# Performance work log

Measured on AMD Instinct MI355X. Metric: run time of the kernel, lower is better.

Reference implementation:

```python
import jax, jax.numpy as jnp
import numpy as np

B, L, S, E, H, Z = 512, 128, 64, 256, 256, 64

def _ln(x, g, b):
    m = jnp.mean(x, -1, keepdims=True)
    v = jnp.mean((x - m) ** 2, -1, keepdims=True)
    return (x - m) / jnp.sqrt(v + 1e-5) * g + b

def _gru_layer(x, Wih, Whh, bih, bhh):
    # x: (B, T, in) -> (outputs (B, T, H), last hidden (B, H)); torch nn.GRU gate math
    xg = jnp.swapaxes(jnp.einsum('bti,gi->btg', x, Wih) + bih, 0, 1)  # (T, B, 3H) precomputed input gates
    h0 = jnp.zeros((x.shape[0], Whh.shape[1]), x.dtype)
    def step(h, xg_t):
        hg = h @ Whh.T + bhh
        xr, xz, xn = jnp.split(xg_t, 3, -1)
        hr, hz, hn = jnp.split(hg, 3, -1)
        r = jax.nn.sigmoid(xr + hr)
        zg = jax.nn.sigmoid(xz + hz)
        n = jnp.tanh(xn + r * hn)
        h_new = (1.0 - zg) * n + zg * h
        return h_new, h_new
    hT, ys = jax.lax.scan(step, h0, xg)
    return jnp.swapaxes(ys, 0, 1), hT

def setup_inputs() -> dict:
    key = jax.random.key(0)
    ks = iter(jax.random.split(key, 64))
    def u(shape, fan):
        s = 1.0 / np.sqrt(fan)
        return jax.random.uniform(next(ks), shape, jnp.float32, -s, s)
    inp = {
        'x': jax.random.normal(next(ks), (B, L, S), jnp.float32),
        'eps': jax.random.normal(next(ks), (B, Z), jnp.float32),
        'dec_noise': jax.random.normal(next(ks), (B, L, Z), jnp.float32),
        'in_W': u((E, S), S), 'in_b': u((E,), S),
        'in_g': jnp.ones((E,), jnp.float32), 'in_beta': jnp.zeros((E,), jnp.float32),
        'eW0i': u((3 * H, E), H), 'eW0h': u((3 * H, H), H), 'eb0i': u((3 * H,), H), 'eb0h': u((3 * H,), H),
        'eW1i': u((3 * H, H), H), 'eW1h': u((3 * H, H), H), 'eb1i': u((3 * H,), H), 'eb1h': u((3 * H,), H),
        'mu_W': u((Z, H), H), 'mu_b': u((Z,), H), 'lv_W': u((Z, H), H), 'lv_b': u((Z,), H),
        'dW0i': u((3 * H, Z), H), 'dW0h': u((3 * H, H), H), 'db0i': u((3 * H,), H), 'db0h': u((3 * H,), H),
        'dW1i': u((3 * H, H), H), 'dW1h': u((3 * H, H), H), 'db1i': u((3 * H,), H), 'db1h': u((3 * H,), H),
        'post_W': u((H, H), H), 'post_b': u((H,), H),
        'post_g': jnp.ones((H,), jnp.float32), 'post_beta': jnp.zeros((H,), jnp.float32),
        'out_W': u((S, H), H), 'out_b': u((S,), H),
    }
    return inp

def reference(x, eps, dec_noise, in_W, in_b, in_g, in_beta,
              eW0i, eW0h, eb0i, eb0h, eW1i, eW1h, eb1i, eb1h,
              mu_W, mu_b, lv_W, lv_b,
              dW0i, dW0h, db0i, db0h, dW1i, dW1h, db1i, db1h,
              post_W, post_b, post_g, post_beta, out_W, out_b):
    # encode
    h = _ln(jax.nn.relu(x @ in_W.T + in_b), in_g, in_beta)          # input_proj
    h, _ = _gru_layer(h, eW0i, eW0h, eb0i, eb0h)                    # encoder GRU layer 0
    _, h_last = _gru_layer(h, eW1i, eW1h, eb1i, eb1h)               # encoder GRU layer 1, h_n[-1]
    mu = h_last @ mu_W.T + mu_b
    log_var = h_last @ lv_W.T + lv_b
    z = mu + eps * jnp.exp(0.5 * log_var)                           # reparameterize
    # decode
    z_seq = jnp.broadcast_to(z[:, None, :], (z.shape[0], L, Z)) + dec_noise * 0.05
    d, _ = _gru_layer(z_seq, dW0i, dW0h, db0i, db0h)
    d, _ = _gru_layer(d, dW1i, dW1h, db1i, db1h)
    d = _ln(jax.nn.relu(d @ post_W.T + post_b), post_g, post_beta)  # post_rnn_proj
    x_hat = jnp.tanh(d @ out_W.T + out_b)                           # output_layer
    return (x_hat, mu, log_var)
```

## Files before the change

kernel.cpp:

```cpp
#include <hip/hip_runtime.h>
#include <hip/hip_bf16.h>
#include <stdint.h>

#define DEVI static __device__ __forceinline__

typedef __bf16 bf16x8 __attribute__((ext_vector_type(8)));
typedef float f32x4 __attribute__((ext_vector_type(4)));
typedef int   int4v __attribute__((ext_vector_type(4)));
typedef int   int2v __attribute__((ext_vector_type(2)));

DEVI float bf2f(uint16_t u){ uint32_t x = ((uint32_t)u) << 16; float f; __builtin_memcpy(&f, &x, 4); return f; }
DEVI uint16_t f2bf(float f){ uint32_t u; __builtin_memcpy(&u, &f, 4); uint32_t r = (u + 0x7FFFu + ((u >> 16) & 1u)) >> 16; return (uint16_t)r; }
DEVI float frcp(float x){ return __builtin_amdgcn_rcpf(x); }
DEVI float sigm(float x){ return frcp(1.f + __expf(-x)); }
DEVI float tanhfast(float x){ return 1.f - 2.f * frcp(1.f + __expf(2.f * x)); }
DEVI f32x4 mfma16(bf16x8 a, bf16x8 b, f32x4 c){ return __builtin_amdgcn_mfma_f32_16x16x32_bf16(a, b, c, 0, 0, 0); }

DEVI bf16x8 cvt8(const float* __restrict__ p){
    f32x4 a = *(const f32x4*)p, b = *(const f32x4*)(p + 4);
    union { bf16x8 v; uint16_t u[8]; } r;
    #pragma unroll
    for (int e = 0; e < 4; ++e) { r.u[e] = f2bf(a[e]); r.u[4 + e] = f2bf(b[e]); }
    return r.v;
}
DEVI int4v asint4(bf16x8 v){ int4v r; __builtin_memcpy(&r, &v, 16); return r; }

DEVI void bar_lds(){
    asm volatile("s_waitcnt lgkmcnt(0)" ::: "memory");
    __builtin_amdgcn_s_barrier();
    __builtin_amdgcn_sched_barrier(0);
}


__global__ __launch_bounds__(256) void k_inproj(
    const float* __restrict__ X, const float* __restrict__ W,
    const float* __restrict__ bias, const float* __restrict__ g,
    const float* __restrict__ beta, uint16_t* __restrict__ Y)
{
    __shared__ __align__(16) char As[64 * 128];
    __shared__ __align__(16) char Bs[256 * 128];
    __shared__ __align__(16) char Cs[64 * 520];
    const int tid = threadIdx.x;
    const long rowbase = (long)blockIdx.x * 64;

    #pragma unroll
    for (int it = 0; it < 2; ++it) {
        int c = it * 256 + tid; int r = c >> 3, cc = c & 7;
        bf16x8 v = cvt8(X + (rowbase + r) * 64 + cc * 8);
        *(int4v*)(As + r * 128 + ((cc * 16) ^ ((r & 7) << 4))) = asint4(v);
    }
    #pragma unroll
    for (int it = 0; it < 8; ++it) {
        int c = it * 256 + tid; int r = c >> 3, cc = c & 7;
        bf16x8 v = cvt8(W + r * 64 + cc * 8);
        *(int4v*)(Bs + r * 128 + ((cc * 16) ^ ((r & 7) << 4))) = asint4(v);
    }
    __syncthreads();

    const int w = tid >> 6, l = tid & 63, lr = l & 15, lg = l >> 4;
    f32x4 acc[16];
    #pragma unroll
    for (int i = 0; i < 16; ++i) acc[i] = (f32x4){0.f, 0.f, 0.f, 0.f};
    const int arow = w * 16 + lr;
    #pragma unroll
    for (int ks = 0; ks < 2; ++ks) {
        bf16x8 a = *(bf16x8*)(As + arow * 128 + ((ks * 64 + lg * 16) ^ ((arow & 7) << 4)));
        #pragma unroll
        for (int tl = 0; tl < 16; ++tl) {
            int n = tl * 16 + lr;
            bf16x8 b = *(bf16x8*)(Bs + n * 128 + ((ks * 64 + lg * 16) ^ ((n & 7) << 4)));
            acc[tl] = mfma16(a, b, acc[tl]);
        }
    }
    float gv[16], bv[16], biasv[16];
    #pragma unroll
    for (int tl = 0; tl < 16; ++tl) {
        int col = tl * 16 + lr;
        gv[tl] = g[col]; bv[tl] = beta[col]; biasv[tl] = bias[col];
    }
    #pragma unroll
    for (int i = 0; i < 4; ++i) {
        float s = 0.f, sq = 0.f, v[16];
        #pragma unroll
        for (int tl = 0; tl < 16; ++tl) {
            float xv = acc[tl][i] + biasv[tl]; xv = fmaxf(xv, 0.f);
            v[tl] = xv; s += xv; sq += xv * xv;
        }
        #pragma unroll
        for (int d = 1; d < 16; d <<= 1) { s += __shfl_xor(s, d); sq += __shfl_xor(sq, d); }
        float mean = s * (1.f / 256.f);
        float var  = sq * (1.f / 256.f) - mean * mean;
        float sc   = rsqrtf(var + 1e-5f);
        int rl = w * 16 + lg * 4 + i;
        #pragma unroll
        for (int tl = 0; tl < 16; ++tl)
            *(uint16_t*)(Cs + rl * 520 + (tl * 16 + lr) * 2) =
                f2bf((v[tl] - mean) * sc * gv[tl] + bv[tl]);
    }
    __syncthreads();
    #pragma unroll
    for (int it = 0; it < 16; ++it) {
        int idx = it * 256 + tid;
        int rl = idx >> 6, ch = idx & 63;
        long rg = rowbase + rl;
        long ri = ((rg & 127) << 9) + (rg >> 7);
        *(int2v*)(Y + ri * 256 + ch * 4) = *(int2v*)(Cs + rl * 520 + ch * 8);
    }
}

template<int KIN, bool ZBUILD>
__global__ __launch_bounds__(512) void k_xg(
    const uint16_t* __restrict__ A, const float* __restrict__ W,
    const float* __restrict__ bias, uint16_t* __restrict__ XG,
    const float* __restrict__ zbuf, const float* __restrict__ noise)
{
    constexpr int KB = KIN * 2;
    constexpr int KS = KIN / 32;
    __shared__ __align__(16) char Bs[192 * KB];
    __shared__ __align__(16) char Cs[128 * 400];
    const int tid = threadIdx.x;
    const int nb = blockIdx.y;

    constexpr int CPR = KIN / 8;
    for (int c = tid; c < 192 * CPR; c += 512) {
        int r = c / CPR, cc = c % CPR;
        bf16x8 v = cvt8(W + (long)(nb * 192 + r) * KIN + cc * 8);
        *(int4v*)(Bs + r * KB + ((cc * 16) ^ ((r & 7) << 4))) = asint4(v);
    }
    __syncthreads();

    const int w = tid >> 6, l = tid & 63, lr = l & 15, lg = l >> 4;
    float bvs[12];
    #pragma unroll
    for (int tl = 0; tl < 12; ++tl) bvs[tl] = bias[nb * 192 + tl * 16 + lr];

    for (int rt = 0; rt < 8; ++rt) {
        const long rowb = (long)blockIdx.x * 1024 + rt * 128;
        const long ria  = rowb + w * 16 + lr;
        bf16x8 a[KS];
        if constexpr (!ZBUILD) {
            #pragma unroll
            for (int ks = 0; ks < KS; ++ks)
                a[ks] = *(const bf16x8*)(A + ria * KIN + ks * 32 + lg * 8);
        } else {
            int b = (int)(ria & 511), t = (int)(ria >> 9);
            #pragma unroll
            for (int ks = 0; ks < KS; ++ks) {
                int k0 = ks * 32 + lg * 8;
                const float* zr = zbuf + b * 64 + k0;
                const float* nr = noise + ((long)b * 128 + t) * 64 + k0;
                f32x4 z0 = *(const f32x4*)zr, z1 = *(const f32x4*)(zr + 4);
                f32x4 n0 = *(const f32x4*)nr, n1 = *(const f32x4*)(nr + 4);
                union { bf16x8 v; uint16_t u[8]; } un;
                #pragma unroll
                for (int e = 0; e < 4; ++e) {
                    un.u[e]     = f2bf(z0[e] + 0.05f * n0[e]);
                    un.u[4 + e] = f2bf(z1[e] + 0.05f * n1[e]);
                }
                a[ks] = un.v;
            }
        }
        f32x4 acc[12];
        #pragma unroll
        for (int i = 0; i < 12; ++i) acc[i] = (f32x4){0.f, 0.f, 0.f, 0.f};
        #pragma unroll
        for (int ks = 0; ks < KS; ++ks) {
            #pragma unroll
            for (int tl = 0; tl < 12; ++tl) {
                int n = tl * 16 + lr;
                bf16x8 b = *(bf16x8*)(Bs + n * KB + ((ks * 64 + lg * 16) ^ ((n & 7) << 4)));
                acc[tl] = mfma16(a[ks], b, acc[tl]);
            }
        }
        #pragma unroll
        for (int tl = 0; tl < 12; ++tl) {
            #pragma unroll
            for (int i = 0; i < 4; ++i)
                *(uint16_t*)(Cs + (w * 16 + lg * 4 + i) * 400 + (tl * 16 + lr) * 2) =
                    f2bf(acc[tl][i] + bvs[tl]);
        }
        __syncthreads();
        #pragma unroll
        for (int it = 0; it < 6; ++it) {
            int idx = it * 512 + tid;
            int row = idx / 24, ch = idx % 24;
            *(int4v*)(XG + (rowb + row) * 768 + nb * 192 + ch * 8) =
                *(int4v*)(Cs + row * 400 + ch * 16);
        }
        __syncthreads();
    }
}

__global__ __launch_bounds__(512) void k_gru(
    const uint16_t* __restrict__ XG, const float* __restrict__ Whh,
    const float* __restrict__ bhh, uint16_t* __restrict__ Y,
    float* __restrict__ hlast)
{
    constexpr int L = 128;
    __shared__ __align__(16) char Abuf[2][2 * 512];
    __shared__ __align__(16) char Wt[768 * 72 + 8];
    const int tid = threadIdx.x;
    const int w = tid >> 6, l = tid & 63, lr = l & 15, lg = l >> 4;
    const int rowg0 = blockIdx.x * 2;

    ((uint32_t*)Abuf)[tid] = 0;

    #pragma unroll
    for (int it = 0; it < 6; ++it) {
        int c = it * 512 + tid; int r = c >> 2, cc = c & 3;
        bf16x8 v = cvt8(Whh + (long)r * 256 + 224 + cc * 8);
        *(int4v*)(Wt + r * 72 + cc * 16) = asint4(v);
    }

    int gb[6];
    #pragma unroll
    for (int tl = 0; tl < 6; ++tl) gb[tl] = (tl >> 1) * 256 + w * 32 + (tl & 1) * 16;
    bf16x8 wf[6][7];
    #pragma unroll
    for (int tl = 0; tl < 6; ++tl)
        #pragma unroll
        for (int ks = 0; ks < 7; ++ks)
            wf[tl][ks] = cvt8(Whh + (long)(gb[tl] + lr) * 256 + ks * 32 + lg * 8);

    const int i_  = lg & 1;
    const int sub = (lg >> 1) & 1;
    const int col = w * 32 + sub * 16 + lr;
    const float bR = bhh[col], bZ = bhh[256 + col], bN = bhh[512 + col];
    const long rowl = rowg0 + i_;
    const int wrbyte = i_ * 512 + ((((col * 2) & ~15) ^ (i_ << 6)) | ((col * 2) & 15));

    uint16_t xga0 = XG[rowl * 768 + col];
    uint16_t xga1 = XG[rowl * 768 + 256 + col];
    uint16_t xga2 = XG[rowl * 768 + 512 + col];
    float h = 0.f;
    const bool wy = (Y != nullptr);
    const int arow = lr & 1;
    __syncthreads();

    for (int t = 0; t < L; ++t) {
        const int p = t & 1;
        f32x4 acc[6];
        #pragma unroll
        for (int i = 0; i < 6; ++i) acc[i] = (f32x4){0.f, 0.f, 0.f, 0.f};

        const char* ab = Abuf[p];
        bf16x8 aq[4];
        #pragma unroll
        for (int i = 0; i < 4; ++i)
            aq[i] = *(bf16x8*)(ab + arow * 512 + ((i * 64 + lg * 16) ^ (arow << 6)));
        #pragma unroll
        for (int ks = 0; ks < 8; ++ks) {
            bf16x8 acur = aq[ks & 3];
            if (ks + 4 < 8)
                aq[ks & 3] = *(bf16x8*)(ab + arow * 512 + (((ks + 4) * 64 + lg * 16) ^ (arow << 6)));
            if (ks < 7) {
                #pragma unroll
                for (int tl = 0; tl < 6; ++tl) acc[tl] = mfma16(acur, wf[tl][ks], acc[tl]);
            } else {
                #pragma unroll
                for (int tl = 0; tl < 6; ++tl) {
                    bf16x8 b = *(bf16x8*)(Wt + (gb[tl] + lr) * 72 + lg * 16);
                    acc[tl] = mfma16(acur, b, acc[tl]);
                }
            }
        }

        float pre0, pre1, pre2;
        {
            float a0 = i_ ? acc[0][1] : acc[0][0];
            float a1 = i_ ? acc[1][1] : acc[1][0];
            pre0 = sub ? a1 : a0;
            float b0 = i_ ? acc[2][1] : acc[2][0];
            float b1 = i_ ? acc[3][1] : acc[3][0];
            pre1 = sub ? b1 : b0;
            float c0 = i_ ? acc[4][1] : acc[4][0];
            float c1 = i_ ? acc[5][1] : acc[5][0];
            pre2 = sub ? c1 : c0;
        }
        float xr = bf2f(xga0), xz = bf2f(xga1), xn = bf2f(xga2);
        float R = sigm(xr + pre0 + bR);
        float Z = sigm(xz + pre1 + bZ);
        float N = tanhfast(xn + R * (pre2 + bN));
        h = N + Z * (h - N);
        uint16_t hb = f2bf(h);
        *(uint16_t*)(Abuf[p ^ 1] + wrbyte) = hb;

        if (t + 1 < L) {
            const uint16_t* src = XG + ((long)(t + 1) * 512 + rowl) * 768;
            xga0 = src[col]; xga1 = src[256 + col]; xga2 = src[512 + col];
        }
        if (wy) Y[((long)t * 512 + rowl) * 256 + col] = hb;
        bar_lds();
    }
    if (hlast) hlast[rowl * 256 + col] = h;
}

__global__ __launch_bounds__(256) void k_z(
    const float* __restrict__ hlast, const float* __restrict__ muW,
    const float* __restrict__ mub, const float* __restrict__ lvW,
    const float* __restrict__ lvb, const float* __restrict__ eps,
    float* __restrict__ mu_out, float* __restrict__ lv_out,
    float* __restrict__ zout)
{
    __shared__ float hrow[2][256];
    __shared__ float res[2][128];
    const int tid = threadIdx.x;
    const long row0 = (long)blockIdx.x * 2;
    for (int i = tid; i < 512; i += 256) ((float*)hrow)[i] = hlast[row0 * 256 + i];
    __syncthreads();
    const int lrr = tid >> 7, c = tid & 127;
    const float* Wr = (c < 64 ? muW : lvW) + (long)(c & 63) * 256;
    float acc = (c < 64) ? mub[c] : lvb[c & 63];
    const float* hr = hrow[lrr];
    #pragma unroll 8
    for (int k = 0; k < 256; k += 4) {
        f32x4 wv = *(const f32x4*)(Wr + k);
        #pragma unroll
        for (int e = 0; e < 4; ++e) acc += hr[k + e] * wv[e];
    }
    res[lrr][c] = acc;
    long row = row0 + lrr;
    if (c < 64) mu_out[row * 64 + c] = acc;
    else        lv_out[row * 64 + (c & 63)] = acc;
    __syncthreads();
    if (c < 64) {
        float m = res[lrr][c], lv = res[lrr][64 + c];
        zout[row * 64 + c] = m + eps[row * 64 + c] * __expf(0.5f * lv);
    }
}

__global__ __launch_bounds__(256) void k_post(
    const uint16_t* __restrict__ D1, const float* __restrict__ pW,
    const float* __restrict__ pb, const float* __restrict__ pg,
    const float* __restrict__ pbeta, const float* __restrict__ oW,
    const float* __restrict__ ob, float* __restrict__ xhat)
{
    __shared__ __align__(16) char Bs[256 * 512];
    const int tid = threadIdx.x;
    const long rowbase = (long)blockIdx.x * 64;
    #pragma unroll
    for (int it = 0; it < 32; ++it) {
        int c = it * 256 + tid; int r = c >> 5, cc = c & 31;
        bf16x8 v = cvt8(pW + r * 256 + cc * 8);
        *(int4v*)(Bs + r * 512 + ((cc * 16) ^ ((r & 7) << 4))) = asint4(v);
    }
    __syncthreads();
    const int w = tid >> 6, l = tid & 63, lr = l & 15, lg = l >> 4;
    const long arow = rowbase + w * 16 + lr;
    bf16x8 af[8];
    #pragma unroll
    for (int ks = 0; ks < 8; ++ks) af[ks] = *(const bf16x8*)(D1 + arow * 256 + ks * 32 + lg * 8);
    f32x4 acc[16];
    #pragma unroll
    for (int i = 0; i < 16; ++i) acc[i] = (f32x4){0.f, 0.f, 0.f, 0.f};
    #pragma unroll
    for (int ks = 0; ks < 8; ++ks) {
        #pragma unroll
        for (int tl = 0; tl < 16; ++tl) {
            int n = tl * 16 + lr;
            bf16x8 b = *(bf16x8*)(Bs + n * 512 + ((ks * 64 + lg * 16) ^ ((n & 7) << 4)));
            acc[tl] = mfma16(af[ks], b, acc[tl]);
        }
    }
    float gv[16], bv[16], biasv[16];
    #pragma unroll
    for (int tl = 0; tl < 16; ++tl) {
        int col = tl * 16 + lr;
        gv[tl] = pg[col]; bv[tl] = pbeta[col]; biasv[tl] = pb[col];
    }
    uint16_t dl[16][4];
    #pragma unroll
    for (int i = 0; i < 4; ++i) {
        float s = 0.f, sq = 0.f, v[16];
        #pragma unroll
        for (int tl = 0; tl < 16; ++tl) {
            float xv = acc[tl][i] + biasv[tl]; xv = fmaxf(xv, 0.f);
            v[tl] = xv; s += xv; sq += xv * xv;
        }
        #pragma unroll
        for (int d = 1; d < 16; d <<= 1) { s += __shfl_xor(s, d); sq += __shfl_xor(sq, d); }
        float mean = s * (1.f / 256.f);
        float var  = sq * (1.f / 256.f) - mean * mean;
        float sc   = rsqrtf(var + 1e-5f);
        #pragma unroll
        for (int tl = 0; tl < 16; ++tl)
            dl[tl][i] = f2bf((v[tl] - mean) * sc * gv[tl] + bv[tl]);
    }
    __syncthreads();
    #pragma unroll
    for (int tl = 0; tl < 16; ++tl) {
        int col = tl * 16 + lr;
        #pragma unroll
        for (int i = 0; i < 4; ++i) {
            int row = w * 16 + lg * 4 + i;
            *(uint16_t*)(Bs + row * 512 + (((col * 2) & ~15) ^ ((row & 7) << 4)) + ((col * 2) & 15)) = dl[tl][i];
        }
    }
    __syncthreads();
    const int ar2 = w * 16 + lr;
    f32x4 acc2[4];
    #pragma unroll
    for (int i = 0; i < 4; ++i) acc2[i] = (f32x4){0.f, 0.f, 0.f, 0.f};
    #pragma unroll
    for (int ks = 0; ks < 8; ++ks) {
        bf16x8 a = *(bf16x8*)(Bs + ar2 * 512 + ((ks * 64 + lg * 16) ^ ((ar2 & 7) << 4)));
        #pragma unroll
        for (int tl = 0; tl < 4; ++tl) {
            int n = tl * 16 + lr;
            bf16x8 b = cvt8(oW + n * 256 + ks * 32 + lg * 8);
            acc2[tl] = mfma16(a, b, acc2[tl]);
        }
    }
    #pragma unroll
    for (int tl = 0; tl < 4; ++tl) {
        int col = tl * 16 + lr;
        float bo = ob[col];
        #pragma unroll
        for (int i = 0; i < 4; ++i) {
            long ri = rowbase + w * 16 + lg * 4 + i;
            long b = ri & 511, t = ri >> 9;
            xhat[(b * 128 + t) * 64 + col] = tanhfast(acc2[tl][i] + bo);
        }
    }
}

extern "C" void kernel_launch(void* const* d_in, const int* in_sizes, int n_in,
                              void* d_out, int out_size, void* d_ws, size_t ws_size,
                              hipStream_t stream)
{
    (void)in_sizes; (void)n_in; (void)out_size; (void)ws_size;
    const float* x     = (const float*)d_in[0];
    const float* eps   = (const float*)d_in[1];
    const float* dnz   = (const float*)d_in[2];
    const float* in_W  = (const float*)d_in[3];
    const float* in_b  = (const float*)d_in[4];
    const float* in_g  = (const float*)d_in[5];
    const float* in_be = (const float*)d_in[6];
    const float* eW0i  = (const float*)d_in[7];
    const float* eW0h  = (const float*)d_in[8];
    const float* eb0i  = (const float*)d_in[9];
    const float* eb0h  = (const float*)d_in[10];
    const float* eW1i  = (const float*)d_in[11];
    const float* eW1h  = (const float*)d_in[12];
    const float* eb1i  = (const float*)d_in[13];
    const float* eb1h  = (const float*)d_in[14];
    const float* mu_W  = (const float*)d_in[15];
    const float* mu_b  = (const float*)d_in[16];
    const float* lv_W  = (const float*)d_in[17];
    const float* lv_b  = (const float*)d_in[18];
    const float* dW0i  = (const float*)d_in[19];
    const float* dW0h  = (const float*)d_in[20];
    const float* db0i  = (const float*)d_in[21];
    const float* db0h  = (const float*)d_in[22];
    const float* dW1i  = (const float*)d_in[23];
    const float* dW1h  = (const float*)d_in[24];
    const float* db1i  = (const float*)d_in[25];
    const float* db1h  = (const float*)d_in[26];
    const float* postW = (const float*)d_in[27];
    const float* postb = (const float*)d_in[28];
    const float* postg = (const float*)d_in[29];
    const float* postbe= (const float*)d_in[30];
    const float* outW  = (const float*)d_in[31];
    const float* outb  = (const float*)d_in[32];

    char* ws = (char*)d_ws;
    uint16_t* XG   = (uint16_t*)(ws);
    uint16_t* YA   = (uint16_t*)(ws + 100663296);
    uint16_t* YB   = (uint16_t*)(ws + 134217728);
    float*    hlast= (float*)   (ws + 167772160);
    float*    zbuf = (float*)   (ws + 168296448);

    float* out    = (float*)d_out;
    float* mu_out = out + 4194304;
    float* lv_out = out + 4194304 + 32768;

    dim3 b256(256), b512(512);
    dim3 gxg(64, 4);

    k_inproj<<<1024, b256, 0, stream>>>(x, in_W, in_b, in_g, in_be, YA);
    k_xg<256,false><<<gxg, b512, 0, stream>>>(YA, eW0i, eb0i, XG, nullptr, nullptr);
    k_gru<<<256, b512, 0, stream>>>(XG, eW0h, eb0h, YB, nullptr);
    k_xg<256,false><<<gxg, b512, 0, stream>>>(YB, eW1i, eb1i, XG, nullptr, nullptr);
    k_gru<<<256, b512, 0, stream>>>(XG, eW1h, eb1h, nullptr, hlast);
    k_z<<<256, b256, 0, stream>>>(hlast, mu_W, mu_b, lv_W, lv_b, eps, mu_out, lv_out, zbuf);
    k_xg<64,true><<<gxg, b512, 0, stream>>>(nullptr, dW0i, db0i, XG, zbuf, dnz);
    k_gru<<<256, b512, 0, stream>>>(XG, dW0h, db0h, YA, nullptr);
    k_xg<256,false><<<gxg, b512, 0, stream>>>(YA, dW1i, db1i, XG, nullptr, nullptr);
    k_gru<<<256, b512, 0, stream>>>(XG, dW1h, db1h, YB, nullptr);
    k_post<<<1024, b256, 0, stream>>>(YB, postW, postb, postg, postbe, outW, outb, out);
}
```

Measured before the change: 955.1 us.

## Add register-resident 4-wave GRU kernel for encoder and fold r/z hidden biases

Adds k_gru4, a 256-thread GRU recurrence kernel that keeps the whole recurrent weight matrix in registers (12x8 bf16 fragments per lane) and computes two hidden columns per lane. This removes the LDS-resident weight slice and its per-step LDS reads that k_gru uses. The encoder layers switch to it, while the decoder layers keep k_gru. Separately, the r and z hidden biases are folded into the precomputed input-gate bias, which saves two adds per step. The cost is very high register pressure with one wave per EU, and only 4 waves per block to hide per-step latency.

```diff
diff --git a/kernel.cpp b/kernel.cpp
--- a/kernel.cpp
+++ b/kernel.cpp
@@ -111,7 +111,8 @@
 template<int KIN, bool ZBUILD>
 __global__ __launch_bounds__(512) void k_xg(
     const uint16_t* __restrict__ A, const float* __restrict__ W,
-    const float* __restrict__ bias, uint16_t* __restrict__ XG,
+    const float* __restrict__ bias, const float* __restrict__ bhh,
+    uint16_t* __restrict__ XG,
     const float* __restrict__ zbuf, const float* __restrict__ noise)
 {
     constexpr int KB = KIN * 2;
@@ -132,7 +133,10 @@
     const int w = tid >> 6, l = tid & 63, lr = l & 15, lg = l >> 4;
     float bvs[12];
     #pragma unroll
-    for (int tl = 0; tl < 12; ++tl) bvs[tl] = bias[nb * 192 + tl * 16 + lr];
+    for (int tl = 0; tl < 12; ++tl) {
+        int colg = nb * 192 + tl * 16 + lr;
+        bvs[tl] = bias[colg] + (colg < 512 ? bhh[colg] : 0.f);
+    }
 
     for (int rt = 0; rt < 8; ++rt) {
         const long rowb = (long)blockIdx.x * 1024 + rt * 128;
@@ -191,6 +195,97 @@
     }
 }
 
+__global__ __launch_bounds__(256)
+__attribute__((amdgpu_waves_per_eu(1, 1)))
+void k_gru4(
+    const uint16_t* __restrict__ XG, const float* __restrict__ Whh,
+    const float* __restrict__ bhh, uint16_t* __restrict__ Y,
+    float* __restrict__ hlast)
+{
+    constexpr int L = 128;
+    __shared__ __align__(16) char Abuf[2][2 * 512];
+    const int tid = threadIdx.x;
+    const int w = tid >> 6, l = tid & 63, lr = l & 15, lg = l >> 4;
+    const int rowg0 = blockIdx.x * 2;
+
+    ((uint32_t*)Abuf)[tid] = 0;
+    ((uint32_t*)Abuf)[256 + tid] = 0;
+
+    int gb[12];
+    #pragma unroll
+    for (int tl = 0; tl < 12; ++tl) gb[tl] = (tl >> 2) * 256 + w * 64 + (tl & 3) * 16;
+    bf16x8 wf[12][8];
+    #pragma unroll
+    for (int tl = 0; tl < 12; ++tl)
+        #pragma unroll
+        for (int ks = 0; ks < 8; ++ks)
+            wf[tl][ks] = cvt8(Whh + (long)(gb[tl] + lr) * 256 + ks * 32 + lg * 8);
+
+    const int row = lg & 1;
+    const int hi  = (lg >> 1) & 1;
+    const int col0 = w * 64 + hi * 32 + lr;
+    const int col1 = col0 + 16;
+    const long rowl = rowg0 + row;
+    const float bN0 = bhh[512 + col0], bN1 = bhh[512 + col1];
+    const int wr0 = row * 512 + ((((col0 * 2) & ~15) ^ (row << 6)) | ((col0 * 2) & 15));
+    const int wr1 = row * 512 + ((((col1 * 2) & ~15) ^ (row << 6)) | ((col1 * 2) & 15));
+
+    uint16_t xr0 = XG[rowl * 768 + col0], xz0 = XG[rowl * 768 + 256 + col0], xn0 = XG[rowl * 768 + 512 + col0];
+    uint16_t xr1 = XG[rowl * 768 + col1], xz1 = XG[rowl * 768 + 256 + col1], xn1 = XG[rowl * 768 + 512 + col1];
+    float h0 = 0.f, h1 = 0.f;
+    const bool wy = (Y != nullptr);
+    const int arow = lr & 1;
+    __syncthreads();
+
+    for (int t = 0; t < L; ++t) {
+        const int p = t & 1;
+        const char* ab = Abuf[p];
+        f32x4 acc[12];
+        #pragma unroll
+        for (int i = 0; i < 12; ++i) acc[i] = (f32x4){0.f, 0.f, 0.f, 0.f};
+        #pragma unroll
+        for (int ks = 0; ks < 8; ++ks) {
+            bf16x8 a = *(bf16x8*)(ab + arow * 512 + ((ks * 64 + lg * 16) ^ (arow << 6)));
+            #pragma unroll
+            for (int tl = 0; tl < 12; ++tl) acc[tl] = mfma16(a, wf[tl][ks], acc[tl]);
+        }
+
+        #define SELG(tA, tB) (hi ? (row ? acc[tB][1] : acc[tB][0]) \
+                                 : (row ? acc[tA][1] : acc[tA][0]))
+        float pR0 = SELG(0, 2),  pR1 = SELG(1, 3);
+        float pZ0 = SELG(4, 6),  pZ1 = SELG(5, 7);
+        float pN0 = SELG(8, 10), pN1 = SELG(9, 11);
+        #undef SELG
+
+        float R0 = sigm(bf2f(xr0) + pR0);
+        float Z0 = sigm(bf2f(xz0) + pZ0);
+        float N0 = tanhfast(bf2f(xn0) + R0 * (pN0 + bN0));
+        h0 = N0 + Z0 * (h0 - N0);
+        float R1 = sigm(bf2f(xr1) + pR1);
+        float Z1 = sigm(bf2f(xz1) + pZ1);
+        float N1 = tanhfast(bf2f(xn1) + R1 * (pN1 + bN1));
+        h1 = N1 + Z1 * (h1 - N1);
+        uint16_t hb0 = f2bf(h0), hb1 = f2bf(h1);
+        *(uint16_t*)(Abuf[p ^ 1] + wr0) = hb0;
+        *(uint16_t*)(Abuf[p ^ 1] + wr1) = hb1;
+
+        if (t + 1 < L) {
+            const uint16_t* src = XG + ((long)(t + 1) * 512 + rowl) * 768;
+            xr0 = src[col0]; xz0 = src[256 + col0]; xn0 = src[512 + col0];
+            xr1 = src[col1]; xz1 = src[256 + col1]; xn1 = src[512 + col1];
+        }
+        if (wy) {
+            uint16_t* yd = Y + ((long)t * 512 + rowl) * 256;
+            yd[col0] = hb0; yd[col1] = hb1;
+        }
+        bar_lds();
+    }
+    if (hlast) {
+        hlast[rowl * 256 + col0] = h0;
+        hlast[rowl * 256 + col1] = h1;
+    }
+}
+
 __global__ __launch_bounds__(512) void k_gru(
     const uint16_t* __restrict__ XG, const float* __restrict__ Whh,
     const float* __restrict__ bhh, uint16_t* __restrict__ Y,
@@ -225,7 +320,7 @@
     const int i_  = lg & 1;
     const int sub = (lg >> 1) & 1;
     const int col = w * 32 + sub * 16 + lr;
-    const float bR = bhh[col], bZ = bhh[256 + col], bN = bhh[512 + col];
+    const float bN = bhh[512 + col];
     const long rowl = rowg0 + i_;
     const int wrbyte = i_ * 512 + ((((col * 2) & ~15) ^ (i_ << 6)) | ((col * 2) & 15));
 
@@ -278,8 +373,8 @@
             pre2 = sub ? c1 : c0;
         }
         float xr = bf2f(xga0), xz = bf2f(xga1), xn = bf2f(xga2);
-        float R = sigm(xr + pre0 + bR);
-        float Z = sigm(xz + pre1 + bZ);
+        float R = sigm(xr + pre0);
+        float Z = sigm(xz + pre1);
         float N = tanhfast(xn + R * (pre2 + bN));
         h = N + Z * (h - N);
         uint16_t hb = f2bf(h);
@@ -478,14 +573,14 @@
     dim3 gxg(64, 4);
 
     k_inproj<<<1024, b256, 0, stream>>>(x, in_W, in_b, in_g, in_be, YA);
-    k_xg<256,false><<<gxg, b512, 0, stream>>>(YA, eW0i, eb0i, XG, nullptr, nullptr);
-    k_gru<<<256, b512, 0, stream>>>(XG, eW0h, eb0h, YB, nullptr);
-    k_xg<256,false><<<gxg, b512, 0, stream>>>(YB, eW1i, eb1i, XG, nullptr, nullptr);
-    k_gru<<<256, b512, 0, stream>>>(XG, eW1h, eb1h, nullptr, hlast);
+    k_xg<256,false><<<gxg, b512, 0, stream>>>(YA, eW0i, eb0i, eb0h, XG, nullptr, nullptr);
+    k_gru4<<<256, b256, 0, stream>>>(XG, eW0h, eb0h, YB, nullptr);
+    k_xg<256,false><<<gxg, b512, 0, stream>>>(YB, eW1i, eb1i, eb1h, XG, nullptr, nullptr);
+    k_gru4<<<256, b256, 0, stream>>>(XG, eW1h, eb1h, nullptr, hlast);
     k_z<<<256, b256, 0, stream>>>(hlast, mu_W, mu_b, lv_W, lv_b, eps, mu_out, lv_out, zbuf);
-    k_xg<64,true><<<gxg, b512, 0, stream>>>(nullptr, dW0i, db0i, XG, zbuf, dnz);
+    k_xg<64,true><<<gxg, b512, 0, stream>>>(nullptr, dW0i, db0i, db0h, XG, zbuf, dnz);
     k_gru<<<256, b512, 0, stream>>>(XG, dW0h, db0h, YA, nullptr);
-    k_xg<256,false><<<gxg, b512, 0, stream>>>(YA, dW1i, db1i, XG, nullptr, nullptr);
+    k_xg<256,false><<<gxg, b512, 0, stream>>>(YA, dW1i, db1i, db1h, XG, nullptr, nullptr);
     k_gru<<<256, b512, 0, stream>>>(XG, dW1h, db1h, YB, nullptr);
     k_post<<<1024, b256, 0, stream>>>(YB, postW, postb, postg, postbe, outW, outb, out);
 }
```

Result: slower. 1.132 ms (+18.5%).
